# Kernel tuning notes

Hardware: AMD Instinct MI355X
Metric: run time of the kernel (lower is better)

The kernel has to match this reference:

```python
import jax, jax.numpy as jnp
import numpy as np

B, T, DIM, HEADS, DH = 4, 2048, 1024, 16, 64
MAX_SEQ_LEN = 2048


def setup_inputs() -> dict:
    key = jax.random.key(0)
    k1, k2, k3, k4 = jax.random.split(key, 4)
    x = jax.random.normal(k1, (B, T, DIM), dtype=jnp.float32)
    W_qkv = jax.random.normal(k2, (DIM, 3 * HEADS * DH), dtype=jnp.float32) * (DIM ** -0.5)
    W_0 = jax.random.normal(k3, (HEADS * DH, DIM), dtype=jnp.float32) * ((HEADS * DH) ** -0.5)
    rel_bias = jax.random.normal(k4, (2 * MAX_SEQ_LEN - 1, HEADS), dtype=jnp.float32) * 0.02
    return {"x": x, "W_qkv": W_qkv, "W_0": W_0, "rel_bias": rel_bias}


def reference(x, W_qkv, W_0, rel_bias):
    b, t, dim = x.shape
    heads = rel_bias.shape[1]
    dh = W_qkv.shape[1] // (3 * heads)
    scale = dh ** -0.5

    qkv = x @ W_qkv  # (b, t, 3*heads*dh), feature layout is (d, k, h): d slowest, h fastest
    qkv = qkv.reshape(b, t, dh, 3, heads)
    qkv = jnp.transpose(qkv, (3, 0, 4, 1, 2))  # (3, b, h, t, d)
    q, k, v = qkv[0], qkv[1], qkv[2]

    scores = jnp.einsum('bhid,bhjd->bhij', q, k) * scale  # (b, h, t, t)

    causal = jnp.tril(jnp.ones((t, t), dtype=bool))
    scores = jnp.where(causal[None, None], scores, -jnp.inf)

    # relative position bias: index = j - i + t - 1
    rel_idx = jnp.arange(t)[None, :] - jnp.arange(t)[:, None] + (t - 1)  # (t, t)
    bias = rel_bias[rel_idx]  # (t, t, heads)
    scores = scores + jnp.transpose(bias, (2, 0, 1))[None]

    attn = jax.nn.softmax(scores, axis=-1)
    out = jnp.einsum('bhij,bhjd->bhid', attn, v)  # (b, h, t, d)
    out = jnp.transpose(out, (0, 2, 1, 3)).reshape(b, t, heads * dh)
    return out @ W_0
```

## Files before the change

### kernel.cpp

```cpp
#include <hip/hip_runtime.h>
#include <hip/hip_bf16.h>
#include <stdint.h>

#define B_ 4
#define T_ 2048
#define NH 16
#define DH 64
#define DIM 1024
#define NF 3072

typedef unsigned short u16;
typedef uint32_t u32;
typedef __bf16 bf16;
typedef bf16 bf16x8 __attribute__((ext_vector_type(8)));
typedef float f32x4 __attribute__((ext_vector_type(4)));
typedef u16 u16x8 __attribute__((ext_vector_type(8)));
typedef u16 u16x4 __attribute__((ext_vector_type(4)));

__device__ __forceinline__ u16 f2bf(float f) {
    u32 u = __builtin_bit_cast(u32, f);
    u = (u + 0x7fffu + ((u >> 16) & 1u)) >> 16;
    return (u16)u;
}

__device__ __forceinline__ float exp2f_fast(float x) {
#if __has_builtin(__builtin_amdgcn_exp2f)
    return __builtin_amdgcn_exp2f(x);
#else
    return exp2f(x);
#endif
}

#define GLOAD16(g, l)                                                          \
    __builtin_amdgcn_global_load_lds(                                          \
        (const __attribute__((address_space(1))) u32*)(g),                     \
        (__attribute__((address_space(3))) u32*)(l), 16, 0, 0)


__global__ __launch_bounds__(256) void cvt_bf16_k(const float* __restrict__ src,
                                                  u16* __restrict__ dst, int n8) {
    int i = blockIdx.x * 256 + threadIdx.x;
    if (i >= n8) return;
    const float4* s = (const float4*)src + (size_t)i * 2;
    float4 a = s[0], b = s[1];
    u16x8 o;
    o[0]=f2bf(a.x); o[1]=f2bf(a.y); o[2]=f2bf(a.z); o[3]=f2bf(a.w);
    o[4]=f2bf(b.x); o[5]=f2bf(b.y); o[6]=f2bf(b.z); o[7]=f2bf(b.w);
    *(u16x8*)(dst + (size_t)i * 8) = o;
}

template <int PERM>
__global__ __launch_bounds__(256) void wcvt_t_k(const float* __restrict__ src,
                                                u16* __restrict__ dst, int K, int N) {
    __shared__ float tile[32][33];
    int n0 = blockIdx.x * 32, k0 = blockIdx.y * 32;
    int c = threadIdx.x & 31, r0 = threadIdx.x >> 5;
#pragma unroll
    for (int i = 0; i < 4; i++) {
        int r = r0 + i * 8;
        tile[r][c] = src[(size_t)(k0 + r) * N + n0 + c];
    }
    __syncthreads();
#pragma unroll
    for (int i = 0; i < 4; i++) {
        int r = r0 + i * 8;
        int n = n0 + r;
        int nd;
        if (PERM) {
            int d = n / 48, rem = n - d * 48;
            int kk = rem >> 4, h = rem & 15;
            nd = kk * 1024 + h * 64 + d;
        } else {
            nd = n;
        }
        dst[(size_t)nd * K + k0 + c] = f2bf(tile[c][r]);
    }
}

__global__ __launch_bounds__(256) void rbt_k(const float* __restrict__ rb,
                                             u16* __restrict__ rbT2,
                                             u16* __restrict__ rbT2s) {
    int i = blockIdx.x * 256 + threadIdx.x;
    if (i >= NH * 4096) return;
    int h = i >> 12, d = i & 4095;
    float v = (d <= 2047) ? rb[(size_t)d * NH + h] * 1.44269504f : -1e30f;
    rbT2[i] = __builtin_bit_cast(u16, (bf16)v);
    int d2 = d + 1;
    float v2 = (d2 <= 2047) ? rb[(size_t)d2 * NH + h] * 1.44269504f : -1e30f;
    rbT2s[i] = __builtin_bit_cast(u16, (bf16)v2);
}

__global__ __launch_bounds__(256) void transpose_v_k(const u16* __restrict__ qkvF,
                                                     u16* __restrict__ Vt) {
    __shared__ __align__(16) u16 tile[64][72];
    int bh = blockIdx.y;
    int h = bh & 15, b = bh >> 4;
    int t0 = blockIdx.x * 64;
    const u16* src = qkvF + ((size_t)b * T_ + t0) * NF + 2048 + h * 64;
    for (int idx = threadIdx.x; idx < 512; idx += 256) {
        int r = idx >> 3, ch = idx & 7;
        *(u16x8*)&tile[r][ch * 8] = *(const u16x8*)&src[(size_t)r * NF + ch * 8];
    }
    __syncthreads();
    u16* dst = Vt + (size_t)bh * DH * T_ + t0;
    for (int idx = threadIdx.x; idx < 512; idx += 256) {
        int d = idx >> 3, ch = idx & 7;
        u16x8 v;
#pragma unroll
        for (int e = 0; e < 8; e++) v[e] = tile[ch * 8 + e][d];
        *(u16x8*)&dst[(size_t)d * T_ + ch * 8] = v;
    }
}


template <int WRITE_BF16>
__global__ __launch_bounds__(256, 2) void gemm_bt_k(const u16* __restrict__ A,
                                                    const u16* __restrict__ Bt,
                                                    void* __restrict__ Cout,
                                                    int M, int N, int K) {
    __shared__ __align__(16) u16 As[128 * 64];
    __shared__ __align__(16) u16 Bs[128 * 64];
    const int tid = threadIdx.x;
    const int wave = tid >> 6, lane = tid & 63;
    const int bm = blockIdx.x, bn = blockIdx.y;
    const int wr = (wave >> 1) * 64, wc = (wave & 1) * 64;
    const int lrow = lane & 15, g4 = lane >> 4;
    const int srow8 = lane >> 3;
    const int scs = (lane & 7) ^ srow8;
    const u16* Ab = A + (size_t)(bm * 128 + wave * 32) * K;
    const u16* Bb = Bt + (size_t)(bn * 128 + wave * 32) * K;
    u16* AsW = As + wave * 2048;
    u16* BsW = Bs + wave * 2048;
    f32x4 acc[4][4] = {};

    for (int k0 = 0; k0 < K; k0 += 64) {
        __syncthreads();
#pragma unroll
        for (int g = 0; g < 4; g++) {
            GLOAD16(Ab + (size_t)(g * 8 + srow8) * K + k0 + scs * 8, AsW + g * 512);
            GLOAD16(Bb + (size_t)(g * 8 + srow8) * K + k0 + scs * 8, BsW + g * 512);
        }
        __syncthreads();
#pragma unroll
        for (int kk2 = 0; kk2 < 2; kk2++) {
            bf16x8 af[4], bfr[4];
#pragma unroll
            for (int i = 0; i < 4; i++)
                af[i] = *(const bf16x8*)&As[(wr + i * 16 + lrow) * 64 +
                                            (((kk2 * 4 + g4) ^ (lrow & 7)) * 8)];
#pragma unroll
            for (int j = 0; j < 4; j++)
                bfr[j] = *(const bf16x8*)&Bs[(wc + j * 16 + lrow) * 64 +
                                             (((kk2 * 4 + g4) ^ (lrow & 7)) * 8)];
#pragma unroll
            for (int i = 0; i < 4; i++)
#pragma unroll
                for (int j = 0; j < 4; j++)
                    acc[i][j] = __builtin_amdgcn_mfma_f32_16x16x32_bf16(af[i], bfr[j],
                                                                        acc[i][j], 0, 0, 0);
        }
    }

    const int crow = (lane >> 4) * 4, ccol = lane & 15;
#pragma unroll
    for (int i = 0; i < 4; i++)
#pragma unroll
        for (int j = 0; j < 4; j++) {
            int gm = bm * 128 + wr + i * 16 + crow;
            int gn = bn * 128 + wc + j * 16 + ccol;
#pragma unroll
            for (int r = 0; r < 4; r++) {
                if (WRITE_BF16)
                    ((u16*)Cout)[(size_t)(gm + r) * N + gn] = f2bf(acc[i][j][r]);
                else
                    ((float*)Cout)[(size_t)(gm + r) * N + gn] = acc[i][j][r];
            }
        }
}

__global__ __launch_bounds__(256, 2) void flash_attn_k(const u16* __restrict__ qkvF,
                                                       const u16* __restrict__ Vt,
                                                       const u16* __restrict__ rbT2,
                                                       const u16* __restrict__ rbT2s,
                                                       u16* __restrict__ O) {
    __shared__ __align__(16) u16 Ks[64 * 64];
    __shared__ __align__(16) u16 Vs[64 * 64];
    __shared__ __align__(16) u16 Ps[4][2][16 * 64];
    __shared__ __align__(16) u16 rbs2a[4096];
    __shared__ __align__(16) u16 rbs2b[4096];
    const int tid = threadIdx.x, wave = tid >> 6, lane = tid & 63;
    const int Lid = blockIdx.x;
    const int c = Lid & 7, u = Lid >> 3;
    const int bh = ((u & 7) << 3) | c;
    const int pair = u >> 3;
    const int h = bh & 15, b = bh >> 4;
    const int l15 = lane & 15, g4 = lane >> 4;
    const float SC2 = 0.125f * 1.44269504f;

    {
        *(u16x8*)&rbs2a[tid * 8] = *(const u16x8*)&rbT2[(size_t)h * 4096 + tid * 8];
        *(u16x8*)&rbs2a[2048 + tid * 8] = *(const u16x8*)&rbT2[(size_t)h * 4096 + 2048 + tid * 8];
        *(u16x8*)&rbs2b[tid * 8] = *(const u16x8*)&rbT2s[(size_t)h * 4096 + tid * 8];
        *(u16x8*)&rbs2b[2048 + tid * 8] = *(const u16x8*)&rbT2s[(size_t)h * 4096 + 2048 + tid * 8];
    }

    const size_t trow = (size_t)b * T_;
    const int srow = tid >> 2;
    const int sch = tid & 3;
    u16* pwA = &Ps[wave][0][0];
    u16* pwB = &Ps[wave][1][0];
    const u16* kgb = &qkvF[(trow + srow) * NF + 1024 + h * 64];
    const u16* vgb = &Vt[((size_t)bh * DH + srow) * T_];

    u16x8 kv0 = *(const u16x8*)&kgb[sch * 8];
    u16x8 kv1 = *(const u16x8*)&kgb[(sch + 4) * 8];
    u16x8 vv0 = *(const u16x8*)&vgb[sch * 8];
    u16x8 vv1 = *(const u16x8*)&vgb[(sch + 4) * 8];

    for (int half = 0; half < 2; half++) {
        const int blk = half ? 15 - pair : pair;
        const int qbA = blk * 128 + wave * 16;
        const int qbB = qbA + 64;
        bf16x8 aqA[2], aqB[2];
        aqA[0] = *(const bf16x8*)&qkvF[(trow + qbA + l15) * NF + h * 64 + g4 * 8];
        aqA[1] = *(const bf16x8*)&qkvF[(trow + qbA + l15) * NF + h * 64 + 32 + g4 * 8];
        aqB[0] = *(const bf16x8*)&qkvF[(trow + qbB + l15) * NF + h * 64 + g4 * 8];
        aqB[1] = *(const bf16x8*)&qkvF[(trow + qbB + l15) * NF + h * 64 + 32 + g4 * 8];

        const int ibA = 2047 - l15 + g4 * 4 - qbA;
        const u32* b32A = (const u32*)((ibA & 1) ? &rbs2b[ibA - 1] : &rbs2a[ibA]);
        const u32* b32B = b32A - 32;

        f32x4 oaccA[4] = {}, oaccB[4] = {};
        float lA = 0.f, lB = 0.f;

        const int jtmax = 2 * blk + 1;
        for (int jt = 0; jt <= jtmax; jt++) {
            const int j0 = jt * 64;
            __syncthreads();
            {
                int sw = srow & 7;
                *(u16x8*)&Ks[srow * 64 + ((sch ^ sw) * 8)] = kv0;
                *(u16x8*)&Ks[srow * 64 + (((sch + 4) ^ sw) * 8)] = kv1;
                *(u16x8*)&Vs[srow * 64 + ((sch ^ sw) * 8)] = vv0;
                *(u16x8*)&Vs[srow * 64 + (((sch + 4) ^ sw) * 8)] = vv1;
            }
            __syncthreads();
            {
                int njt = jt + 1;
                int j0n = (njt <= jtmax) ? njt * 64 : (half == 0 ? 0 : -1);
                if (j0n >= 0) {
                    const u16* kg = kgb + (size_t)j0n * NF;
                    const u16* vg = vgb + j0n;
                    kv0 = *(const u16x8*)&kg[sch * 8];
                    kv1 = *(const u16x8*)&kg[(sch + 4) * 8];
                    vv0 = *(const u16x8*)&vg[sch * 8];
                    vv1 = *(const u16x8*)&vg[(sch + 4) * 8];
                }
            }
            f32x4 sA[4], sB[4];
#pragma unroll
            for (int ni = 0; ni < 4; ni++) {
                f32x4 z = {};
                sA[ni] = z;
                sB[ni] = z;
            }
            __builtin_amdgcn_s_setprio(1);
#pragma unroll
            for (int ni = 0; ni < 4; ni++) {
                int arow = ni * 16 + l15;
#pragma unroll
                for (int kk = 0; kk < 2; kk++) {
                    int ch = kk * 4 + g4;
                    bf16x8 ak = *(const bf16x8*)&Ks[arow * 64 + ((ch ^ (arow & 7)) * 8)];
                    sA[ni] = __builtin_amdgcn_mfma_f32_16x16x32_bf16(ak, aqA[kk], sA[ni], 0, 0, 0);
                    sB[ni] = __builtin_amdgcn_mfma_f32_16x16x32_bf16(ak, aqB[kk], sB[ni], 0, 0, 0);
                }
            }
            __builtin_amdgcn_s_setprio(0);
            const int jo = j0 >> 1;
            {
                float su = 0.f;
#pragma unroll
                for (int ni = 0; ni < 4; ni++) {
                    u32 w0 = b32A[jo + ni * 8];
                    u32 w1 = b32A[jo + ni * 8 + 1];
                    float e0 = exp2f_fast(fmaf(sA[ni][0], SC2, __builtin_bit_cast(float, w0 << 16)));
                    float e1 = exp2f_fast(fmaf(sA[ni][1], SC2, __builtin_bit_cast(float, w0 & 0xffff0000u)));
                    float e2 = exp2f_fast(fmaf(sA[ni][2], SC2, __builtin_bit_cast(float, w1 << 16)));
                    float e3 = exp2f_fast(fmaf(sA[ni][3], SC2, __builtin_bit_cast(float, w1 & 0xffff0000u)));
                    su += (e0 + e1) + (e2 + e3);
                    u16x4 pk;
                    pk[0] = __builtin_bit_cast(u16, (bf16)e0);
                    pk[1] = __builtin_bit_cast(u16, (bf16)e1);
                    pk[2] = __builtin_bit_cast(u16, (bf16)e2);
                    pk[3] = __builtin_bit_cast(u16, (bf16)e3);
                    int colb = ni * 16 + g4 * 4;
                    int ch = colb >> 3, co = colb & 7;
                    *(u16x4*)&pwA[l15 * 64 + ((ch ^ (l15 & 7)) * 8) + co] = pk;
                }
                su += __shfl_xor(su, 16);
                su += __shfl_xor(su, 32);
                lA += su;
            }
            {
                float su = 0.f;
#pragma unroll
                for (int ni = 0; ni < 4; ni++) {
                    u32 w0 = b32B[jo + ni * 8];
                    u32 w1 = b32B[jo + ni * 8 + 1];
                    float e0 = exp2f_fast(fmaf(sB[ni][0], SC2, __builtin_bit_cast(float, w0 << 16)));
                    float e1 = exp2f_fast(fmaf(sB[ni][1], SC2, __builtin_bit_cast(float, w0 & 0xffff0000u)));
                    float e2 = exp2f_fast(fmaf(sB[ni][2], SC2, __builtin_bit_cast(float, w1 << 16)));
                    float e3 = exp2f_fast(fmaf(sB[ni][3], SC2, __builtin_bit_cast(float, w1 & 0xffff0000u)));
                    su += (e0 + e1) + (e2 + e3);
                    u16x4 pk;
                    pk[0] = __builtin_bit_cast(u16, (bf16)e0);
                    pk[1] = __builtin_bit_cast(u16, (bf16)e1);
                    pk[2] = __builtin_bit_cast(u16, (bf16)e2);
                    pk[3] = __builtin_bit_cast(u16, (bf16)e3);
                    int colb = ni * 16 + g4 * 4;
                    int ch = colb >> 3, co = colb & 7;
                    *(u16x4*)&pwB[l15 * 64 + ((ch ^ (l15 & 7)) * 8) + co] = pk;
                }
                su += __shfl_xor(su, 16);
                su += __shfl_xor(su, 32);
                lB += su;
            }
            bf16x8 bpA[2], bpB[2];
#pragma unroll
            for (int kk = 0; kk < 2; kk++) {
                int ch = kk * 4 + g4;
                int off = l15 * 64 + ((ch ^ (l15 & 7)) * 8);
                bpA[kk] = *(const bf16x8*)&pwA[off];
                bpB[kk] = *(const bf16x8*)&pwB[off];
            }
            __builtin_amdgcn_s_setprio(1);
#pragma unroll
            for (int di = 0; di < 4; di++) {
                int vrow = di * 16 + l15;
#pragma unroll
                for (int kk = 0; kk < 2; kk++) {
                    int ch = kk * 4 + g4;
                    bf16x8 av = *(const bf16x8*)&Vs[vrow * 64 + ((ch ^ (vrow & 7)) * 8)];
                    oaccA[di] = __builtin_amdgcn_mfma_f32_16x16x32_bf16(av, bpA[kk], oaccA[di], 0, 0, 0);
                    oaccB[di] = __builtin_amdgcn_mfma_f32_16x16x32_bf16(av, bpB[kk], oaccB[di], 0, 0, 0);
                }
            }
            __builtin_amdgcn_s_setprio(0);
        }
        {
            float inv = 1.0f / lA;
            u16* orow = &O[((size_t)b * T_ + qbA + l15) * (NH * DH) + h * DH];
#pragma unroll
            for (int di = 0; di < 4; di++) {
                u16x4 ov;
#pragma unroll
                for (int r = 0; r < 4; r++)
                    ov[r] = __builtin_bit_cast(u16, (bf16)(oaccA[di][r] * inv));
                *(u16x4*)&orow[di * 16 + g4 * 4] = ov;
            }
        }
        {
            float inv = 1.0f / lB;
            u16* orow = &O[((size_t)b * T_ + qbB + l15) * (NH * DH) + h * DH];
#pragma unroll
            for (int di = 0; di < 4; di++) {
                u16x4 ov;
#pragma unroll
                for (int r = 0; r < 4; r++)
                    ov[r] = __builtin_bit_cast(u16, (bf16)(oaccB[di][r] * inv));
                *(u16x4*)&orow[di * 16 + g4 * 4] = ov;
            }
        }
    }
}


extern "C" void kernel_launch(void* const* d_in, const int* in_sizes, int n_in,
                              void* d_out, int out_size, void* d_ws, size_t ws_size,
                              hipStream_t stream) {
    const float* x    = (const float*)d_in[0];
    const float* Wqkv = (const float*)d_in[1];
    const float* W0   = (const float*)d_in[2];
    const float* rb   = (const float*)d_in[3];
    char* ws = (char*)d_ws;

    u16*   xb    = (u16*)(ws + 0);
    u16*   WqkvT = (u16*)(ws + 16777216);
    u16*   W0T   = (u16*)(ws + 23068672);
    u16*   rbT2  = (u16*)(ws + 25165824);
    u16*   rbT2s = (u16*)(ws + 25296896);
    u16*   qkvF  = (u16*)(ws + 25559040);
    u16*   attnO = (u16*)(ws + 75890688);
    u16*   Vtb   = (u16*)(ws + 0);

    cvt_bf16_k<<<4096, 256, 0, stream>>>(x, xb, (B_ * T_ * DIM) / 8);
    wcvt_t_k<1><<<dim3(NF / 32, DIM / 32), 256, 0, stream>>>(Wqkv, WqkvT, DIM, NF);
    wcvt_t_k<0><<<dim3(DIM / 32, DIM / 32), 256, 0, stream>>>(W0, W0T, DIM, DIM);
    rbt_k<<<(NH * 4096 + 255) / 256, 256, 0, stream>>>(rb, rbT2, rbT2s);

    gemm_bt_k<1><<<dim3((B_ * T_) / 128, NF / 128), 256, 0, stream>>>(
        xb, WqkvT, qkvF, B_ * T_, NF, DIM);

    transpose_v_k<<<dim3(T_ / 64, B_ * NH), 256, 0, stream>>>(qkvF, Vtb);

    flash_attn_k<<<512, 256, 0, stream>>>(qkvF, Vtb, rbT2, rbT2s, attnO);

    gemm_bt_k<0><<<dim3((B_ * T_) / 128, DIM / 128), 256, 0, stream>>>(
        attnO, W0T, d_out, B_ * T_, DIM, DIM);
}
```

Baseline: 182.2 us.

## Fuse V transpose into QKV GEMM epilogue via swapped-operand MFMA

Splits the QKV projection into a Q/K GEMM writing a 2048-wide buffer and a separate V GEMM whose epilogue writes V directly in transposed (b,h,d,t) layout. The V GEMM swaps the MFMA operands so each lane holds consecutive t values. This removes the standalone transpose kernel and its extra read/write of V. The transposed-store epilogue writes 2-byte elements scattered across rows, which may coalesce poorly, and the V GEMM launches as a small separate grid.

```diff
diff --git a/kernel.cpp b/kernel.cpp
--- a/kernel.cpp
+++ b/kernel.cpp
@@ -8,6 +8,7 @@
 #define DH 64
 #define DIM 1024
 #define NF 3072
+#define QKS 2048
 
 typedef unsigned short u16;
 typedef uint32_t u32;
@@ -90,30 +91,8 @@
     rbT2s[i] = __builtin_bit_cast(u16, (bf16)v2);
 }
 
-__global__ __launch_bounds__(256) void transpose_v_k(const u16* __restrict__ qkvF,
-                                                     u16* __restrict__ Vt) {
-    __shared__ __align__(16) u16 tile[64][72];
-    int bh = blockIdx.y;
-    int h = bh & 15, b = bh >> 4;
-    int t0 = blockIdx.x * 64;
-    const u16* src = qkvF + ((size_t)b * T_ + t0) * NF + 2048 + h * 64;
-    for (int idx = threadIdx.x; idx < 512; idx += 256) {
-        int r = idx >> 3, ch = idx & 7;
-        *(u16x8*)&tile[r][ch * 8] = *(const u16x8*)&src[(size_t)r * NF + ch * 8];
-    }
-    __syncthreads();
-    u16* dst = Vt + (size_t)bh * DH * T_ + t0;
-    for (int idx = threadIdx.x; idx < 512; idx += 256) {
-        int d = idx >> 3, ch = idx & 7;
-        u16x8 v;
-#pragma unroll
-        for (int e = 0; e < 8; e++) v[e] = tile[ch * 8 + e][d];
-        *(u16x8*)&dst[(size_t)d * T_ + ch * 8] = v;
-    }
-}
-
-
-template <int WRITE_BF16>
+
+template <int OUTMODE>
 __global__ __launch_bounds__(256, 2) void gemm_bt_k(const u16* __restrict__ A,
                                                     const u16* __restrict__ Bt,
                                                     void* __restrict__ Cout,
@@ -155,30 +134,53 @@
 #pragma unroll
             for (int i = 0; i < 4; i++)
 #pragma unroll
-                for (int j = 0; j < 4; j++)
-                    acc[i][j] = __builtin_amdgcn_mfma_f32_16x16x32_bf16(af[i], bfr[j],
-                                                                        acc[i][j], 0, 0, 0);
+                for (int j = 0; j < 4; j++) {
+                    if (OUTMODE == 2)
+                        acc[i][j] = __builtin_amdgcn_mfma_f32_16x16x32_bf16(
+                            bfr[j], af[i], acc[i][j], 0, 0, 0);
+                    else
+                        acc[i][j] = __builtin_amdgcn_mfma_f32_16x16x32_bf16(
+                            af[i], bfr[j], acc[i][j], 0, 0, 0);
+                }
         }
     }
 
     const int crow = (lane >> 4) * 4, ccol = lane & 15;
-#pragma unroll
-    for (int i = 0; i < 4; i++)
-#pragma unroll
-        for (int j = 0; j < 4; j++) {
-            int gm = bm * 128 + wr + i * 16 + crow;
-            int gn = bn * 128 + wc + j * 16 + ccol;
-#pragma unroll
-            for (int r = 0; r < 4; r++) {
-                if (WRITE_BF16)
-                    ((u16*)Cout)[(size_t)(gm + r) * N + gn] = f2bf(acc[i][j][r]);
-                else
-                    ((float*)Cout)[(size_t)(gm + r) * N + gn] = acc[i][j][r];
-            }
-        }
-}
-
-__global__ __launch_bounds__(256, 2) void flash_attn_k(const u16* __restrict__ qkvF,
+    if (OUTMODE == 2) {
+        u16* Vt = (u16*)Cout;
+#pragma unroll
+        for (int i = 0; i < 4; i++)
+#pragma unroll
+            for (int j = 0; j < 4; j++) {
+                int gm = bm * 128 + wr + i * 16 + ccol;
+                int b = gm >> 11, tt = gm & 2047;
+#pragma unroll
+                for (int r = 0; r < 4; r++) {
+                    int f = bn * 128 + wc + j * 16 + crow + r;
+                    int h = f >> 6, d = f & 63;
+                    Vt[(((size_t)(b * NH + h)) * DH + d) * T_ + tt] =
+                        f2bf(acc[i][j][r]);
+                }
+            }
+    } else {
+#pragma unroll
+        for (int i = 0; i < 4; i++)
+#pragma unroll
+            for (int j = 0; j < 4; j++) {
+                int gm = bm * 128 + wr + i * 16 + crow;
+                int gn = bn * 128 + wc + j * 16 + ccol;
+#pragma unroll
+                for (int r = 0; r < 4; r++) {
+                    if (OUTMODE == 1)
+                        ((u16*)Cout)[(size_t)(gm + r) * N + gn] = f2bf(acc[i][j][r]);
+                    else
+                        ((float*)Cout)[(size_t)(gm + r) * N + gn] = acc[i][j][r];
+                }
+            }
+    }
+}
+
+__global__ __launch_bounds__(256, 2) void flash_attn_k(const u16* __restrict__ qkF,
                                                        const u16* __restrict__ Vt,
                                                        const u16* __restrict__ rbT2,
                                                        const u16* __restrict__ rbT2s,
@@ -209,7 +211,7 @@
     const int sch = tid & 3;
     u16* pwA = &Ps[wave][0][0];
     u16* pwB = &Ps[wave][1][0];
-    const u16* kgb = &qkvF[(trow + srow) * NF + 1024 + h * 64];
+    const u16* kgb = &qkF[(trow + srow) * QKS + 1024 + h * 64];
     const u16* vgb = &Vt[((size_t)bh * DH + srow) * T_];
 
     u16x8 kv0 = *(const u16x8*)&kgb[sch * 8];
@@ -222,10 +224,10 @@
         const int qbA = blk * 128 + wave * 16;
         const int qbB = qbA + 64;
         bf16x8 aqA[2], aqB[2];
-        aqA[0] = *(const bf16x8*)&qkvF[(trow + qbA + l15) * NF + h * 64 + g4 * 8];
-        aqA[1] = *(const bf16x8*)&qkvF[(trow + qbA + l15) * NF + h * 64 + 32 + g4 * 8];
-        aqB[0] = *(const bf16x8*)&qkvF[(trow + qbB + l15) * NF + h * 64 + g4 * 8];
-        aqB[1] = *(const bf16x8*)&qkvF[(trow + qbB + l15) * NF + h * 64 + 32 + g4 * 8];
+        aqA[0] = *(const bf16x8*)&qkF[(trow + qbA + l15) * QKS + h * 64 + g4 * 8];
+        aqA[1] = *(const bf16x8*)&qkF[(trow + qbA + l15) * QKS + h * 64 + 32 + g4 * 8];
+        aqB[0] = *(const bf16x8*)&qkF[(trow + qbB + l15) * QKS + h * 64 + g4 * 8];
+        aqB[1] = *(const bf16x8*)&qkF[(trow + qbB + l15) * QKS + h * 64 + 32 + g4 * 8];
 
         const int ibA = 2047 - l15 + g4 * 4 - qbA;
         const u32* b32A = (const u32*)((ibA & 1) ? &rbs2b[ibA - 1] : &rbs2a[ibA]);
@@ -250,7 +252,7 @@
                 int njt = jt + 1;
                 int j0n = (njt <= jtmax) ? njt * 64 : (half == 0 ? 0 : -1);
                 if (j0n >= 0) {
-                    const u16* kg = kgb + (size_t)j0n * NF;
+                    const u16* kg = kgb + (size_t)j0n * QKS;
                     const u16* vg = vgb + j0n;
                     kv0 = *(const u16x8*)&kg[sch * 8];
                     kv1 = *(const u16x8*)&kg[(sch + 4) * 8];
@@ -391,21 +393,22 @@
     u16*   W0T   = (u16*)(ws + 23068672);
     u16*   rbT2  = (u16*)(ws + 25165824);
     u16*   rbT2s = (u16*)(ws + 25296896);
-    u16*   qkvF  = (u16*)(ws + 25559040);
-    u16*   attnO = (u16*)(ws + 75890688);
-    u16*   Vtb   = (u16*)(ws + 0);
+    u16*   qkF   = (u16*)(ws + 25427968);
+    u16*   attnO = (u16*)(ws + 58982400);
+    u16*   Vtb   = (u16*)(ws + 75759616);
 
     cvt_bf16_k<<<4096, 256, 0, stream>>>(x, xb, (B_ * T_ * DIM) / 8);
     wcvt_t_k<1><<<dim3(NF / 32, DIM / 32), 256, 0, stream>>>(Wqkv, WqkvT, DIM, NF);
     wcvt_t_k<0><<<dim3(DIM / 32, DIM / 32), 256, 0, stream>>>(W0, W0T, DIM, DIM);
     rbt_k<<<(NH * 4096 + 255) / 256, 256, 0, stream>>>(rb, rbT2, rbT2s);
 
-    gemm_bt_k<1><<<dim3((B_ * T_) / 128, NF / 128), 256, 0, stream>>>(
-        xb, WqkvT, qkvF, B_ * T_, NF, DIM);
-
-    transpose_v_k<<<dim3(T_ / 64, B_ * NH), 256, 0, stream>>>(qkvF, Vtb);
-
-    flash_attn_k<<<512, 256, 0, stream>>>(qkvF, Vtb, rbT2, rbT2s, attnO);
+    gemm_bt_k<1><<<dim3((B_ * T_) / 128, QKS / 128), 256, 0, stream>>>(
+        xb, WqkvT, qkF, B_ * T_, QKS, DIM);
+
+    gemm_bt_k<2><<<dim3((B_ * T_) / 128, (NF - QKS) / 128), 256, 0, stream>>>(
+        xb, WqkvT + (size_t)QKS * DIM, Vtb, B_ * T_, NF - QKS, DIM);
+
+    flash_attn_k<<<512, 256, 0, stream>>>(qkF, Vtb, rbT2, rbT2s, attnO);
 
     gemm_bt_k<0><<<dim3((B_ * T_) / 128, DIM / 128), 256, 0, stream>>>(
         attnO, W0T, d_out, B_ * T_, DIM, DIM);
```

Measured after the change: 177.9 us. 1.02x faster.
